# Kernel optimization log

Measured on AMD Instinct MI355X. Metric: run time of the kernel, lower is better.

The kernel has to match this reference:

```python
import jax, jax.numpy as jnp
import numpy as np

B, S, D = 2, 2048, 1024
H, L = 16, 512
DH = D // H
LN_EPS = 1e-5


def setup_inputs() -> dict:
    key = jax.random.key(0)
    ks = jax.random.split(key, 6)
    w = 0.02  # init scale for weights
    return {
        "x": jax.random.normal(ks[0], (B, S, D), jnp.float32),
        "W_q": jax.random.normal(ks[1], (D, D), jnp.float32) * w,
        "W_dkv": jax.random.normal(ks[2], (L, D), jnp.float32) * w,
        "W_uk": jax.random.normal(ks[3], (D, L), jnp.float32) * w,
        "W_uv": jax.random.normal(ks[4], (D, L), jnp.float32) * w,
        "W_o": jax.random.normal(ks[5], (D, D), jnp.float32) * w,
        "ln_gamma": jnp.ones((L,), jnp.float32),
        "ln_beta": jnp.zeros((L,), jnp.float32),
    }


def reference(x, W_q, W_dkv, W_uk, W_uv, W_o, ln_gamma, ln_beta):
    # latent KV: LayerNorm(x @ W_dkv^T)  -> [B, S, L]
    c = x @ W_dkv.T
    mu = jnp.mean(c, axis=-1, keepdims=True)
    var = jnp.mean((c - mu) ** 2, axis=-1, keepdims=True)
    c_kv = (c - mu) * jax.lax.rsqrt(var + LN_EPS) * ln_gamma + ln_beta

    # absorbed key projection: (W_q @ W_uk) viewed per head  -> [H, DH, L]
    absorbed_k = (W_q @ W_uk).reshape(H, DH, L)

    # q is raw x reshaped per head (W_q absorbed)  -> [B, S, H, DH]
    q = x.reshape(B, S, H, DH)
    tmp = jnp.einsum('bshd,hdl->bhsl', q, absorbed_k)         # [B,H,S,L]
    scores = jnp.einsum('bhsl,btl->bhst', tmp, c_kv) / np.sqrt(DH)

    # causal mask (past_length = 0, no kv_cache -> S_full == S)
    mask = jnp.tril(jnp.ones((S, S), bool))
    scores = jnp.where(mask[None, None], scores, -1e30)
    attn = jax.nn.softmax(scores, axis=-1)                    # [B,H,S,S]

    # values decompressed from latent  -> [B, S, H, DH]
    v = (c_kv @ W_uv.T).reshape(B, S, H, DH)
    ctx = jnp.einsum('bhst,bthd->bshd', attn, v).reshape(B, S, D)
    out = ctx @ W_o.T
    return out, c_kv
```

## Files before the change

### kernel.cpp

```cpp
#include <hip/hip_runtime.h>


typedef __attribute__((ext_vector_type(4))) float f32x4;
typedef __attribute__((ext_vector_type(8))) unsigned short u16x8;
typedef __attribute__((ext_vector_type(4))) unsigned short u16x4;
typedef __attribute__((ext_vector_type(8))) __bf16 bf16x8;

__device__ __forceinline__ unsigned short f2bf(float f) {
  unsigned int u = __builtin_bit_cast(unsigned int, f);
  u += 0x7FFFu + ((u >> 16) & 1u);
  return (unsigned short)(u >> 16);
}
__device__ __forceinline__ unsigned short f2bf_rz(float f) {
  return (unsigned short)(__builtin_bit_cast(unsigned int, f) >> 16);
}
__device__ __forceinline__ float bf2f(unsigned short u) {
  return __builtin_bit_cast(float, (unsigned int)u << 16);
}

__device__ __forceinline__ f32x4 mfma16(u16x8 a, u16x8 b, f32x4 c) {
  return __builtin_amdgcn_mfma_f32_16x16x32_bf16(
      __builtin_bit_cast(bf16x8, a), __builtin_bit_cast(bf16x8, b), c, 0, 0, 0);
}

__device__ __forceinline__ void gload_lds16(const void* g, void* l) {
  __builtin_amdgcn_global_load_lds(
      (const __attribute__((address_space(1))) unsigned int*)g,
      (__attribute__((address_space(3))) unsigned int*)l, 16, 0, 0);
}

__global__ __launch_bounds__(256)
void fused_cvt(const float* __restrict__ x, unsigned short* __restrict__ xb,
               const float* __restrict__ wq, unsigned short* __restrict__ wqb,
               const float* __restrict__ wdkv, unsigned short* __restrict__ wdkvb,
               const float* __restrict__ wuv, unsigned short* __restrict__ wuvb,
               const float* __restrict__ wo, unsigned short* __restrict__ wob,
               const float* __restrict__ wuk, unsigned short* __restrict__ wukT) {
  __shared__ float t[64][65];
  if (blockIdx.x >= 2048) {
    int bid = blockIdx.x - 2048;
    int c0 = (bid & 7) * 64;
    int r0 = (bid >> 3) * 64;
    int lr = threadIdx.x >> 4, lc = (threadIdx.x & 15) * 4;
#pragma unroll
    for (int i = 0; i < 4; i++) {
      int row = lr + i * 16;
      float4 v = *(const float4*)(wuk + (size_t)(r0 + row) * 512 + c0 + lc);
      t[row][lc] = v.x; t[row][lc + 1] = v.y; t[row][lc + 2] = v.z; t[row][lc + 3] = v.w;
    }
    __syncthreads();
#pragma unroll
    for (int i = 0; i < 4; i++) {
      int oc = lr + i * 16;
      u16x4 o;
      o[0] = f2bf(t[lc + 0][oc]); o[1] = f2bf(t[lc + 1][oc]);
      o[2] = f2bf(t[lc + 2][oc]); o[3] = f2bf(t[lc + 3][oc]);
      *(u16x4*)(wukT + (size_t)(c0 + oc) * 1024 + r0 + lc) = o;
    }
    return;
  }
  const int total = 1048576 + 262144 + 131072 + 131072 + 262144;
  for (int i = blockIdx.x * 256 + threadIdx.x; i < total; i += 2048 * 256) {
    const float* src; unsigned short* dst; int off;
    if (i < 1048576)      { src = x;    dst = xb;    off = i; }
    else if (i < 1310720) { src = wq;   dst = wqb;   off = i - 1048576; }
    else if (i < 1441792) { src = wdkv; dst = wdkvb; off = i - 1310720; }
    else if (i < 1572864) { src = wuv;  dst = wuvb;  off = i - 1441792; }
    else                  { src = wo;   dst = wob;   off = i - 1572864; }
    float4 v = ((const float4*)src)[off];
    u16x4 o;
    o[0] = f2bf(v.x); o[1] = f2bf(v.y); o[2] = f2bf(v.z); o[3] = f2bf(v.w);
    ((u16x4*)dst)[off] = o;
  }
}

template <int MODE, int IM, int JF>
__device__ __forceinline__
void gemm_dev(int bx, int by,
              const unsigned short* __restrict__ A, const unsigned short* __restrict__ B,
              void* __restrict__ C1, void* __restrict__ C2,
              int K, int lda, int ldb, int ldc,
              unsigned short* sA, unsigned short* sB) {
  constexpr int BM = IM * 32, BN = JF * 32;
  const int tid = threadIdx.x;
  const int w = tid >> 6, ln = tid & 63;
  const int m0 = by * BM, n0 = bx * BN;
  const int wm = (w >> 1) * (IM * 16), wn = (w & 1) * (JF * 16);
  const int c16 = ln & 15, g = ln >> 4;
  f32x4 zero = {0.f, 0.f, 0.f, 0.f};
  f32x4 acc[IM][JF];
#pragma unroll
  for (int i = 0; i < IM; i++)
#pragma unroll
    for (int j = 0; j < JF; j++) acc[i][j] = zero;

#define STAGE_G(kt, bf)                                                         \
  {                                                                             \
    _Pragma("unroll") for (int l = 0; l < BM / 32; l++) {                       \
      int c = l * 256 + tid;                                                    \
      int row = c >> 3, pc = c & 7;                                             \
      gload_lds16(A + (size_t)(m0 + row) * lda + (kt) + ((pc ^ (row & 7)) << 3),\
                  (char*)(sA + (bf) * (BM * 64)) + (l * 256 + w * 64) * 16);    \
    }                                                                           \
    _Pragma("unroll") for (int l = 0; l < BN / 32; l++) {                       \
      int c = l * 256 + tid;                                                    \
      int row = c >> 3, pc = c & 7;                                             \
      gload_lds16(B + (size_t)(n0 + row) * ldb + (kt) + ((pc ^ (row & 7)) << 3),\
                  (char*)(sB + (bf) * (BN * 64)) + (l * 256 + w * 64) * 16);    \
    }                                                                           \
  }

  STAGE_G(0, 0);
  __syncthreads();
  int bf = 0;
  for (int kt = 0; kt < K; kt += 64) {
    if (kt + 64 < K) STAGE_G(kt + 64, bf ^ 1);
    u16x8 af[IM][2], bfr[JF][2];
#pragma unroll
    for (int i = 0; i < IM; i++) {
      int ra = wm + i * 16 + c16;
#pragma unroll
      for (int kk = 0; kk < 2; kk++)
        af[i][kk] = *(const u16x8*)((const char*)(sA + bf * (BM * 64)) + ra * 128 +
                                    ((((kk << 2) + g) ^ (ra & 7)) << 4));
    }
#pragma unroll
    for (int j = 0; j < JF; j++) {
      int rb = wn + j * 16 + c16;
#pragma unroll
      for (int kk = 0; kk < 2; kk++)
        bfr[j][kk] = *(const u16x8*)((const char*)(sB + bf * (BN * 64)) + rb * 128 +
                                     ((((kk << 2) + g) ^ (rb & 7)) << 4));
    }
#pragma unroll
    for (int kk = 0; kk < 2; kk++)
#pragma unroll
      for (int i = 0; i < IM; i++)
#pragma unroll
        for (int j = 0; j < JF; j++)
          acc[i][j] = mfma16(af[i][kk], bfr[j][kk], acc[i][j]);
    __syncthreads();
    bf ^= 1;
  }
#undef STAGE_G
  const int row0 = m0 + wm + g * 4;
  const int col0 = n0 + wn + c16;
  if (MODE == 1) {
    float* C = (float*)C1;
#pragma unroll
    for (int i = 0; i < IM; i++)
#pragma unroll
      for (int j = 0; j < JF; j++)
#pragma unroll
        for (int r = 0; r < 4; r++)
          C[(size_t)(row0 + i * 16 + r) * ldc + col0 + j * 16] = acc[i][j][r];
  } else if (MODE == 0) {
    unsigned short* C = (unsigned short*)C1;
#pragma unroll
    for (int i = 0; i < IM; i++)
#pragma unroll
      for (int j = 0; j < JF; j++)
#pragma unroll
        for (int r = 0; r < 4; r++)
          C[(size_t)(row0 + i * 16 + r) * ldc + col0 + j * 16] = f2bf(acc[i][j][r]);
  } else {
    if (n0 < 1024) {
      unsigned short* C = (unsigned short*)C1;
#pragma unroll
      for (int i = 0; i < IM; i++)
#pragma unroll
        for (int j = 0; j < JF; j++)
#pragma unroll
          for (int r = 0; r < 4; r++)
            C[(size_t)(row0 + i * 16 + r) * ldc + col0 + j * 16] = f2bf(acc[i][j][r]);
    } else {
      unsigned short* C = (unsigned short*)C2;
#pragma unroll
      for (int i = 0; i < IM; i++)
#pragma unroll
        for (int j = 0; j < JF; j++) {
          u16x4 t4;
#pragma unroll
          for (int r = 0; r < 4; r++) t4[r] = f2bf(acc[i][j][r]);
          *(u16x4*)(C + (size_t)(col0 + j * 16 - 1024) * 4096 + row0 + i * 16) = t4;
        }
    }
  }
}

template <int MODE, int IM, int JF, int MINW>
__global__ __launch_bounds__(256, MINW)
void gemm_bt(const unsigned short* __restrict__ A, const unsigned short* __restrict__ B,
             void* __restrict__ C1, void* __restrict__ C2,
             int K, int lda, int ldb, int ldc) {
  __shared__ __align__(16) unsigned short sA[2 * IM * 32 * 64];
  __shared__ __align__(16) unsigned short sB[2 * JF * 32 * 64];
  gemm_dev<MODE, IM, JF>(blockIdx.x, blockIdx.y, A, B, C1, C2, K, lda, ldb, ldc,
                         sA, sB);
}

__global__ __launch_bounds__(256, 4)
void lnak(const float* __restrict__ cin, const float* __restrict__ gamma,
          const float* __restrict__ beta, float* __restrict__ of32,
          unsigned short* __restrict__ obf,
          const unsigned short* __restrict__ wqb,
          const unsigned short* __restrict__ wukT,
          unsigned short* __restrict__ akt) {
  __shared__ __align__(16) unsigned short sh[2 * 32 * 64 + 2 * 64 * 64];
  if (blockIdx.x >= 1024) {
    int b2 = blockIdx.x - 1024;
    gemm_dev<0, 1, 2>(b2 & 7, b2 >> 3, wqb, wukT, akt, nullptr,
                      1024, 1024, 1024, 512, sh, sh + 2 * 32 * 64);
    return;
  }
  int row = blockIdx.x * 4 + (threadIdx.x >> 6);
  int ln = threadIdx.x & 63;
  const float* r = cin + (size_t)row * 512 + ln * 8;
  float4 a = *(const float4*)r;
  float4 b = *(const float4*)(r + 4);
  float xv[8] = {a.x, a.y, a.z, a.w, b.x, b.y, b.z, b.w};
  float s = 0.f, q = 0.f;
#pragma unroll
  for (int j = 0; j < 8; j++) { s += xv[j]; q += xv[j] * xv[j]; }
#pragma unroll
  for (int m = 1; m < 64; m <<= 1) { s += __shfl_xor(s, m); q += __shfl_xor(q, m); }
  float mu = s * (1.f / 512.f);
  float var = q * (1.f / 512.f) - mu * mu;
  float rs = rsqrtf(var + 1e-5f);
  float gm[8], bt[8];
  *(float4*)&gm[0] = *(const float4*)(gamma + ln * 8);
  *(float4*)&gm[4] = *(const float4*)(gamma + ln * 8 + 4);
  *(float4*)&bt[0] = *(const float4*)(beta + ln * 8);
  *(float4*)&bt[4] = *(const float4*)(beta + ln * 8 + 4);
  float o[8];
#pragma unroll
  for (int j = 0; j < 8; j++) o[j] = (xv[j] - mu) * rs * gm[j] + bt[j];
  float4 o0 = {o[0], o[1], o[2], o[3]}, o1 = {o[4], o[5], o[6], o[7]};
  *(float4*)(of32 + (size_t)row * 512 + ln * 8) = o0;
  *(float4*)(of32 + (size_t)row * 512 + ln * 8 + 4) = o1;
  u16x8 ob;
#pragma unroll
  for (int j = 0; j < 8; j++) ob[j] = f2bf(o[j]);
  *(u16x8*)(obf + (size_t)row * 512 + ln * 8) = ob;
}

__global__ __launch_bounds__(512, 3)
void mla_attn8(const unsigned short* __restrict__ kabs,
               const unsigned short* __restrict__ xq,
               const unsigned short* __restrict__ vT,
               unsigned short* __restrict__ Opart,
               float* __restrict__ Lpart) {
  __shared__ __align__(16) unsigned short sK[2][64 * 64];
  __shared__ __align__(16) unsigned short sVT[2][64 * 64];
  __shared__ __align__(16) unsigned short sP[8][16 * 40];
  const int tid = threadIdx.x, w = tid >> 6, ln = tid & 63;
  const int g = ln >> 4, c16 = ln & 15;
  const int bh = blockIdx.y;
  const int b = bh >> 4, h = bh & 15;
  int cid = blockIdx.x, qb2, ch;
  if (cid < 4)       { qb2 = cid;                  ch = 0; }
  else if (cid < 12) { qb2 = 4 + ((cid - 4) >> 1);   ch = (cid - 4) & 1; }
  else if (cid < 24) { qb2 = 8 + (cid - 12) / 3;     ch = (cid - 12) % 3; }
  else               { qb2 = 12 + ((cid - 24) >> 2); ch = (cid - 24) & 3; }
  const int ts = ch * 8;
  const int te = min(ts + 8, 2 * qb2 + 2);
  const int q0 = qb2 * 128;
  const int qw = q0 + w * 16;
  const size_t rowb = (size_t)b * 2048;

  u16x8 qf[2];
  {
    const unsigned short* qp = xq + (rowb + qw + c16) * 1024 + h * 64 + g * 8;
    qf[0] = *(const u16x8*)(qp);
    qf[1] = *(const u16x8*)(qp + 32);
  }
  f32x4 zero = {0.f, 0.f, 0.f, 0.f};
  f32x4 o[4] = {zero, zero, zero, zero};
  float lsum[4] = {0.f, 0.f, 0.f, 0.f};
  const float SC = 0.18033688011112042f;
  const float M0 = 8.f;
  unsigned short* Pw = &sP[w][0];
  const unsigned short* kb_g = kabs + rowb * 1024 + h * 64;
  const unsigned short* vb_g = vT + (size_t)(h * 64) * 4096 + rowb;
  const int srow = tid >> 3, spc = tid & 7;

#define STAGE_A(tt, bfi)                                                        \
  {                                                                             \
    int t0s = (tt) * 64;                                                        \
    gload_lds16(kb_g + (size_t)(t0s + srow) * 1024 + ((spc ^ (srow & 7)) << 3), \
                (char*)&sK[bfi][0] + (w << 10));                                \
    gload_lds16(vb_g + (size_t)srow * 4096 + t0s + ((spc ^ (srow & 7)) << 3),   \
                (char*)&sVT[bfi][0] + (w << 10));                               \
  }

  STAGE_A(ts, 0);
  __syncthreads();
  int bf = 0;
  for (int tt = ts; tt < te; tt++) {
    const int t0 = tt * 64;
    if (tt + 1 < te) STAGE_A(tt + 1, bf ^ 1);
    f32x4 s[4];
#pragma unroll
    for (int nt = 0; nt < 4; nt++) {
      int t = nt * 16 + c16;
      int sw = t & 7;
      const char* kb = (const char*)&sK[bf][0] + t * 128;
      f32x4 a = zero;
      a = mfma16(qf[0], *(const u16x8*)(kb + ((g ^ sw) << 4)), a);
      a = mfma16(qf[1], *(const u16x8*)(kb + (((4 + g) ^ sw) << 4)), a);
      s[nt] = a;
    }
    if (t0 + 63 <= qw) {
#pragma unroll
      for (int nt = 0; nt < 4; nt++)
#pragma unroll
        for (int r = 0; r < 4; r++) {
          float p = exp2f(s[nt][r] * SC - M0);
          lsum[r] += p;
          s[nt][r] = p;
        }
    } else {
#pragma unroll
      for (int nt = 0; nt < 4; nt++) {
        int tcol = t0 + nt * 16 + c16;
#pragma unroll
        for (int r = 0; r < 4; r++) {
          float p = (tcol <= qw + g * 4 + r) ? exp2f(s[nt][r] * SC - M0) : 0.f;
          lsum[r] += p;
          s[nt][r] = p;
        }
      }
    }
#pragma unroll
    for (int half = 0; half < 2; half++) {
#pragma unroll
      for (int ntl = 0; ntl < 2; ntl++)
#pragma unroll
        for (int r = 0; r < 4; r++)
          Pw[(g * 4 + r) * 40 + ntl * 16 + c16] = f2bf_rz(s[half * 2 + ntl][r]);
      u16x8 pa = *(const u16x8*)((const char*)Pw + c16 * 80 + g * 16);
#pragma unroll
      for (int dt = 0; dt < 4; dt++) {
        int d = dt * 16 + c16;
        const char* vb = (const char*)&sVT[bf][0] + d * 128 +
                         ((((half << 2) + g) ^ (d & 7)) << 4);
        o[dt] = mfma16(pa, *(const u16x8*)vb, o[dt]);
      }
    }
    __syncthreads();
    bf ^= 1;
  }
#undef STAGE_A
  unsigned short* op = Opart + ((size_t)bh * 40 + cid) * 8192;
  float* lp = Lpart + ((size_t)bh * 40 + cid) * 128;
#pragma unroll
  for (int r = 0; r < 4; r++) {
    float t = lsum[r];
    t += __shfl_xor(t, 1); t += __shfl_xor(t, 2);
    t += __shfl_xor(t, 4); t += __shfl_xor(t, 8);
    int ql = w * 16 + g * 4 + r;
    if (c16 == 0) lp[ql] = t;
#pragma unroll
    for (int dt = 0; dt < 4; dt++)
      op[ql * 64 + dt * 16 + c16] = f2bf(o[dt][r]);
  }
}

__global__ __launch_bounds__(512)
void attn_combine(const unsigned short* __restrict__ Opart,
                  const float* __restrict__ Lpart,
                  unsigned short* __restrict__ ctx) {
  const int qb2 = blockIdx.x, bh = blockIdx.y;
  const int b = bh >> 4, h = bh & 15;
  const int ncq = (qb2 >> 2) + 1;
  const int gg = qb2 >> 2;
  const int start = (gg == 0 ? 0 : (gg == 1 ? 4 : (gg == 2 ? 12 : 24)));
  const int cid0 = start + (qb2 & 3) * ncq;
  const int q = threadIdx.x >> 2;
  const int d0 = (threadIdx.x & 3) * 16;
  float acc[16];
#pragma unroll
  for (int j = 0; j < 16; j++) acc[j] = 0.f;
  float lacc = 0.f;
  for (int c = 0; c < ncq; c++) {
    size_t base = (size_t)bh * 40 + cid0 + c;
    lacc += Lpart[base * 128 + q];
    const unsigned short* op = Opart + base * 8192 + q * 64 + d0;
    u16x8 v0 = *(const u16x8*)(op);
    u16x8 v1 = *(const u16x8*)(op + 8);
#pragma unroll
    for (int j = 0; j < 8; j++) { acc[j] += bf2f(v0[j]); acc[8 + j] += bf2f(v1[j]); }
  }
  float inv = 1.f / lacc;
  u16x8 o0, o1;
#pragma unroll
  for (int j = 0; j < 8; j++) { o0[j] = f2bf(acc[j] * inv); o1[j] = f2bf(acc[8 + j] * inv); }
  unsigned short* cp = ctx + ((size_t)b * 2048 + qb2 * 128 + q) * 1024 + h * 64 + d0;
  *(u16x8*)(cp) = o0;
  *(u16x8*)(cp + 8) = o1;
}

extern "C" void kernel_launch(void* const* d_in, const int* in_sizes, int n_in,
                              void* d_out, int out_size, void* d_ws, size_t ws_size,
                              hipStream_t stream) {
  const float* x    = (const float*)d_in[0];
  const float* Wq   = (const float*)d_in[1];
  const float* Wdkv = (const float*)d_in[2];
  const float* Wuk  = (const float*)d_in[3];
  const float* Wuv  = (const float*)d_in[4];
  const float* Wo   = (const float*)d_in[5];
  const float* gam  = (const float*)d_in[6];
  const float* bet  = (const float*)d_in[7];
  float* out_f = (float*)d_out;
  float* ckv_f = out_f + (size_t)4096 * 1024;

  char* ws = (char*)d_ws;
  unsigned short* xb     = (unsigned short*)(ws);
  unsigned short* wq_b   = (unsigned short*)(ws + 8388608);
  unsigned short* wdkv_b = (unsigned short*)(ws + 10485760);
  unsigned short* wukT_b = (unsigned short*)(ws + 11534336);
  unsigned short* akt_b  = (unsigned short*)(ws + 12582912);
  unsigned short* wuv_b  = (unsigned short*)(ws + 13631488);
  unsigned short* wo_b   = (unsigned short*)(ws + 14680064);
  unsigned short* ckv_b  = (unsigned short*)(ws + 16777216);
  float*          c_f    = (float*)(ws + 20971520);
  unsigned short* kabs   = (unsigned short*)(ws + 29360128);
  unsigned short* vT     = (unsigned short*)(ws + 37748736);
  unsigned short* ctx_b  = (unsigned short*)(ws + 46137344);
  unsigned short* Opart  = (unsigned short*)(ws + 54525952);
  float*          Lpart  = (float*)(ws + 75497472);

  fused_cvt<<<2176, 256, 0, stream>>>(x, xb, Wq, wq_b, Wdkv, wdkv_b,
                                      Wuv, wuv_b, Wo, wo_b, Wuk, wukT_b);
  gemm_bt<1, 2, 2, 4><<<dim3(8, 64), 256, 0, stream>>>(xb, wdkv_b, c_f, nullptr,
                                                       1024, 1024, 1024, 512);
  lnak<<<1280, 256, 0, stream>>>(c_f, gam, bet, ckv_f, ckv_b, wq_b, wukT_b, akt_b);
  gemm_bt<3, 4, 4, 2><<<dim3(16, 32), 256, 0, stream>>>(ckv_b, akt_b, kabs, vT,
                                                        512, 512, 512, 1024);
  mla_attn8<<<dim3(40, 32), 512, 0, stream>>>(kabs, xb, vT, Opart, Lpart);
  attn_combine<<<dim3(16, 32), 512, 0, stream>>>(Opart, Lpart, ctx_b);
  gemm_bt<1, 2, 4, 3><<<dim3(8, 64), 256, 0, stream>>>(ctx_b, wo_b, out_f, nullptr,
                                                       1024, 1024, 1024, 1024);
}
```

Measured before the change: 195.7 us.

## Process two query subtiles per wave in attention and fold softmax scale into absorbed key

The attention kernel now runs 4 waves (256 threads) per block, and each wave handles 32 query rows as two 16-row subtiles that share the K and V fragments read from LDS. This halves LDS fragment reads per MFMA and spreads the tile staging over fewer threads with two loads each. The softmax scale is folded into the absorbed-key GEMM epilogue (new MODE 4), which removes a multiply per score. In exchange each thread holds more registers, and there are fewer waves per block to hide latency.

```diff
diff --git a/kernel.cpp b/kernel.cpp
--- a/kernel.cpp
+++ b/kernel.cpp
@@ -163,6 +163,17 @@
 #pragma unroll
         for (int r = 0; r < 4; r++)
           C[(size_t)(row0 + i * 16 + r) * ldc + col0 + j * 16] = f2bf(acc[i][j][r]);
+  } else if (MODE == 4) {
+    const float SCK = 0.18033688011112042f;
+    unsigned short* C = (unsigned short*)C1;
+#pragma unroll
+    for (int i = 0; i < IM; i++)
+#pragma unroll
+      for (int j = 0; j < JF; j++)
+#pragma unroll
+        for (int r = 0; r < 4; r++)
+          C[(size_t)(row0 + i * 16 + r) * ldc + col0 + j * 16] =
+              f2bf(acc[i][j][r] * SCK);
   } else {
     if (n0 < 1024) {
       unsigned short* C = (unsigned short*)C1;
@@ -209,7 +220,7 @@
   __shared__ __align__(16) unsigned short sh[2 * 32 * 64 + 2 * 64 * 64];
   if (blockIdx.x >= 1024) {
     int b2 = blockIdx.x - 1024;
-    gemm_dev<0, 1, 2>(b2 & 7, b2 >> 3, wqb, wukT, akt, nullptr,
+    gemm_dev<4, 1, 2>(b2 & 7, b2 >> 3, wqb, wukT, akt, nullptr,
                       1024, 1024, 1024, 512, sh, sh + 2 * 32 * 64);
     return;
   }
@@ -244,15 +255,15 @@
   *(u16x8*)(obf + (size_t)row * 512 + ln * 8) = ob;
 }
 
-__global__ __launch_bounds__(512, 3)
-void mla_attn8(const unsigned short* __restrict__ kabs,
+__global__ __launch_bounds__(256, 4)
+void mla_attn9(const unsigned short* __restrict__ kabs,
                const unsigned short* __restrict__ xq,
                const unsigned short* __restrict__ vT,
                unsigned short* __restrict__ Opart,
                float* __restrict__ Lpart) {
   __shared__ __align__(16) unsigned short sK[2][64 * 64];
   __shared__ __align__(16) unsigned short sVT[2][64 * 64];
-  __shared__ __align__(16) unsigned short sP[8][16 * 40];
+  __shared__ __align__(16) unsigned short sP[4][16 * 40];
   const int tid = threadIdx.x, w = tid >> 6, ln = tid & 63;
   const int g = ln >> 4, c16 = ln & 15;
   const int bh = blockIdx.y;
@@ -265,32 +276,42 @@
   const int ts = ch * 8;
   const int te = min(ts + 8, 2 * qb2 + 2);
   const int q0 = qb2 * 128;
-  const int qw = q0 + w * 16;
+  const int qw = q0 + w * 32;
   const size_t rowb = (size_t)b * 2048;
 
-  u16x8 qf[2];
+  u16x8 qfA[2], qfB[2];
   {
     const unsigned short* qp = xq + (rowb + qw + c16) * 1024 + h * 64 + g * 8;
-    qf[0] = *(const u16x8*)(qp);
-    qf[1] = *(const u16x8*)(qp + 32);
+    qfA[0] = *(const u16x8*)(qp);
+    qfA[1] = *(const u16x8*)(qp + 32);
+    qfB[0] = *(const u16x8*)(qp + 16 * 1024);
+    qfB[1] = *(const u16x8*)(qp + 16 * 1024 + 32);
   }
   f32x4 zero = {0.f, 0.f, 0.f, 0.f};
-  f32x4 o[4] = {zero, zero, zero, zero};
-  float lsum[4] = {0.f, 0.f, 0.f, 0.f};
-  const float SC = 0.18033688011112042f;
+  f32x4 oA[4] = {zero, zero, zero, zero};
+  f32x4 oB[4] = {zero, zero, zero, zero};
+  float lsA[4] = {0.f, 0.f, 0.f, 0.f};
+  float lsB[4] = {0.f, 0.f, 0.f, 0.f};
   const float M0 = 8.f;
   unsigned short* Pw = &sP[w][0];
   const unsigned short* kb_g = kabs + rowb * 1024 + h * 64;
   const unsigned short* vb_g = vT + (size_t)(h * 64) * 4096 + rowb;
-  const int srow = tid >> 3, spc = tid & 7;
-
-#define STAGE_A(tt, bfi)                                                        \
-  {                                                                             \
-    int t0s = (tt) * 64;                                                        \
-    gload_lds16(kb_g + (size_t)(t0s + srow) * 1024 + ((spc ^ (srow & 7)) << 3), \
-                (char*)&sK[bfi][0] + (w << 10));                                \
-    gload_lds16(vb_g + (size_t)srow * 4096 + t0s + ((spc ^ (srow & 7)) << 3),   \
-                (char*)&sVT[bfi][0] + (w << 10));                               \
+
+#define STAGE_A(tt, bfi)                                                       \
+  {                                                                            \
+    int t0s = (tt) * 64;                                                       \
+    _Pragma("unroll") for (int l = 0; l < 2; l++) {                            \
+      int c = l * 256 + tid;                                                   \
+      int row = c >> 3, pc = c & 7;                                            \
+      gload_lds16(kb_g + (size_t)(t0s + row) * 1024 + ((pc ^ (row & 7)) << 3), \
+                  (char*)&sK[bfi][0] + (l * 256 + w * 64) * 16);               \
+    }                                                                          \
+    _Pragma("unroll") for (int l = 0; l < 2; l++) {                            \
+      int c = l * 256 + tid;                                                   \
+      int row = c >> 3, pc = c & 7;                                            \
+      gload_lds16(vb_g + (size_t)row * 4096 + t0s + ((pc ^ (row & 7)) << 3),   \
+                  (char*)&sVT[bfi][0] + (l * 256 + w * 64) * 16);              \
+    }                                                                          \
   }
 
   STAGE_A(ts, 0);
@@ -299,25 +320,30 @@
   for (int tt = ts; tt < te; tt++) {
     const int t0 = tt * 64;
     if (tt + 1 < te) STAGE_A(tt + 1, bf ^ 1);
-    f32x4 s[4];
+    f32x4 sA[4], sB[4];
 #pragma unroll
     for (int nt = 0; nt < 4; nt++) {
       int t = nt * 16 + c16;
       int sw = t & 7;
       const char* kb = (const char*)&sK[bf][0] + t * 128;
-      f32x4 a = zero;
-      a = mfma16(qf[0], *(const u16x8*)(kb + ((g ^ sw) << 4)), a);
-      a = mfma16(qf[1], *(const u16x8*)(kb + (((4 + g) ^ sw) << 4)), a);
-      s[nt] = a;
+      u16x8 kf0 = *(const u16x8*)(kb + ((g ^ sw) << 4));
+      u16x8 kf1 = *(const u16x8*)(kb + (((4 + g) ^ sw) << 4));
+      f32x4 a = mfma16(qfA[0], kf0, zero);
+      a = mfma16(qfA[1], kf1, a);
+      sA[nt] = a;
+      f32x4 bb = mfma16(qfB[0], kf0, zero);
+      bb = mfma16(qfB[1], kf1, bb);
+      sB[nt] = bb;
     }
     if (t0 + 63 <= qw) {
 #pragma unroll
       for (int nt = 0; nt < 4; nt++)
 #pragma unroll
         for (int r = 0; r < 4; r++) {
-          float p = exp2f(s[nt][r] * SC - M0);
-          lsum[r] += p;
-          s[nt][r] = p;
+          float pA = exp2f(sA[nt][r] - M0);
+          float pB = exp2f(sB[nt][r] - M0);
+          lsA[r] += pA; lsB[r] += pB;
+          sA[nt][r] = pA; sB[nt][r] = pB;
         }
     } else {
 #pragma unroll
@@ -325,9 +351,11 @@
         int tcol = t0 + nt * 16 + c16;
 #pragma unroll
         for (int r = 0; r < 4; r++) {
-          float p = (tcol <= qw + g * 4 + r) ? exp2f(s[nt][r] * SC - M0) : 0.f;
-          lsum[r] += p;
-          s[nt][r] = p;
+          int qg = qw + g * 4 + r;
+          float pA = (tcol <= qg) ? exp2f(sA[nt][r] - M0) : 0.f;
+          float pB = (tcol <= qg + 16) ? exp2f(sB[nt][r] - M0) : 0.f;
+          lsA[r] += pA; lsB[r] += pB;
+          sA[nt][r] = pA; sB[nt][r] = pB;
         }
       }
     }
@@ -337,14 +365,22 @@
       for (int ntl = 0; ntl < 2; ntl++)
 #pragma unroll
         for (int r = 0; r < 4; r++)
-          Pw[(g * 4 + r) * 40 + ntl * 16 + c16] = f2bf_rz(s[half * 2 + ntl][r]);
-      u16x8 pa = *(const u16x8*)((const char*)Pw + c16 * 80 + g * 16);
+          Pw[(g * 4 + r) * 40 + ntl * 16 + c16] = f2bf_rz(sA[half * 2 + ntl][r]);
+      u16x8 paA = *(const u16x8*)((const char*)Pw + c16 * 80 + g * 16);
+#pragma unroll
+      for (int ntl = 0; ntl < 2; ntl++)
+#pragma unroll
+        for (int r = 0; r < 4; r++)
+          Pw[(g * 4 + r) * 40 + ntl * 16 + c16] = f2bf_rz(sB[half * 2 + ntl][r]);
+      u16x8 paB = *(const u16x8*)((const char*)Pw + c16 * 80 + g * 16);
 #pragma unroll
       for (int dt = 0; dt < 4; dt++) {
         int d = dt * 16 + c16;
         const char* vb = (const char*)&sVT[bf][0] + d * 128 +
                          ((((half << 2) + g) ^ (d & 7)) << 4);
-        o[dt] = mfma16(pa, *(const u16x8*)vb, o[dt]);
+        u16x8 vf = *(const u16x8*)vb;
+        oA[dt] = mfma16(paA, vf, oA[dt]);
+        oB[dt] = mfma16(paB, vf, oB[dt]);
       }
     }
     __syncthreads();
@@ -355,14 +391,19 @@
   float* lp = Lpart + ((size_t)bh * 40 + cid) * 128;
 #pragma unroll
   for (int r = 0; r < 4; r++) {
-    float t = lsum[r];
-    t += __shfl_xor(t, 1); t += __shfl_xor(t, 2);
-    t += __shfl_xor(t, 4); t += __shfl_xor(t, 8);
-    int ql = w * 16 + g * 4 + r;
-    if (c16 == 0) lp[ql] = t;
-#pragma unroll
-    for (int dt = 0; dt < 4; dt++)
-      op[ql * 64 + dt * 16 + c16] = f2bf(o[dt][r]);
+    float tA = lsA[r], tB = lsB[r];
+    tA += __shfl_xor(tA, 1); tA += __shfl_xor(tA, 2);
+    tA += __shfl_xor(tA, 4); tA += __shfl_xor(tA, 8);
+    tB += __shfl_xor(tB, 1); tB += __shfl_xor(tB, 2);
+    tB += __shfl_xor(tB, 4); tB += __shfl_xor(tB, 8);
+    int qlA = w * 32 + g * 4 + r;
+    int qlB = qlA + 16;
+    if (c16 == 0) { lp[qlA] = tA; lp[qlB] = tB; }
+#pragma unroll
+    for (int dt = 0; dt < 4; dt++) {
+      op[qlA * 64 + dt * 16 + c16] = f2bf(oA[dt][r]);
+      op[qlB * 64 + dt * 16 + c16] = f2bf(oB[dt][r]);
+    }
   }
 }
 
@@ -437,7 +478,7 @@
   lnak<<<1280, 256, 0, stream>>>(c_f, gam, bet, ckv_f, ckv_b, wq_b, wukT_b, akt_b);
   gemm_bt<3, 4, 4, 2><<<dim3(16, 32), 256, 0, stream>>>(ckv_b, akt_b, kabs, vT,
                                                         512, 512, 512, 1024);
-  mla_attn8<<<dim3(40, 32), 512, 0, stream>>>(kabs, xb, vT, Opart, Lpart);
+  mla_attn9<<<dim3(40, 32), 256, 0, stream>>>(kabs, xb, vT, Opart, Lpart);
   attn_combine<<<dim3(16, 32), 512, 0, stream>>>(Opart, Lpart, ctx_b);
   gemm_bt<1, 2, 4, 3><<<dim3(8, 64), 256, 0, stream>>>(ctx_b, wo_b, out_f, nullptr,
                                                        1024, 1024, 1024, 1024);
```

Measured after the change: 231.8 us. +18.5%, slower.
